# Kernel tuning notes

Hardware: AMD Instinct MI355X
Metric: run time of the kernel (lower is better)

## Reference

```python
import jax, jax.numpy as jnp
import numpy as np

_SAMPLING_EPS = 1e-5
_NEG_INF = -jnp.inf


def _apply_min_p(logits, min_p):
    # probs >= min_p * max_prob are kept (vLLM apply_min_p)
    probs = jax.nn.softmax(logits, axis=-1)
    max_p = jnp.max(probs, axis=-1, keepdims=True)
    keep = probs >= (min_p[:, None] * max_p)
    return jnp.where(keep, logits, _NEG_INF)


def _apply_top_k_top_p(logits, top_k, top_p):
    # One descending sort serves both filters (mirrors vLLM topk/topp kernel).
    T, V = logits.shape
    sorted_l = jnp.sort(logits, axis=-1)[:, ::-1]  # [T, V] descending
    # top-k threshold: k-th largest logit; top_k <= 0 means disabled
    k = jnp.where(top_k <= 0, V, jnp.clip(top_k, 1, V)).astype(jnp.int32)
    kth = jnp.take_along_axis(sorted_l, (k - 1)[:, None], axis=-1)  # [T, 1]
    # top-p: keep smallest prefix whose prob mass reaches top_p (first token always kept)
    probs = jax.nn.softmax(sorted_l, axis=-1)
    cum = jnp.cumsum(probs, axis=-1)
    keep_p = (cum - probs) < top_p[:, None]
    pth = jnp.min(jnp.where(keep_p, sorted_l, jnp.inf), axis=-1, keepdims=True)
    keep = (logits >= kth) & (logits >= pth)
    return jnp.where(keep, logits, _NEG_INF)


def _gather_logprobs(logprobs, num_logprobs, token_ids):
    # vLLM gather_logprobs: topk + sampled-token logprob + rank
    topk_lp, topk_idx = jax.lax.top_k(logprobs, num_logprobs)  # [T, K]
    tok = token_ids[:, None]  # [T, 1]
    tok_lp = jnp.take_along_axis(logprobs, tok, axis=-1)  # [T, 1]
    ranks = jnp.sum(logprobs >= tok_lp, axis=-1).astype(jnp.int32)  # [T]
    indices = jnp.concatenate([tok, topk_idx], axis=1).astype(jnp.int32)
    lps = jnp.concatenate([tok_lp, topk_lp], axis=1)
    return indices, lps, ranks


def setup_inputs() -> dict:
    key = jax.random.key(0)
    k1, k2, k3, k4, k5, k6 = jax.random.split(key, 6)
    T, V = 256, 128256
    logits = jax.random.normal(k1, (T, V), dtype=jnp.float32)
    temperature = 0.2 + 1.3 * jax.random.uniform(k2, (T,), dtype=jnp.float32)
    # every 8th request is greedy (temperature < _SAMPLING_EPS path)
    temperature = jnp.where(jnp.arange(T) % 8 == 0, 0.0, temperature)
    min_p = 0.05 * jax.random.uniform(k3, (T,), dtype=jnp.float32)
    top_p = 0.5 + 0.5 * jax.random.uniform(k4, (T,), dtype=jnp.float32)
    top_k = jax.random.randint(k5, (T,), 0, 64, dtype=jnp.int32)
    u = jax.random.uniform(k6, (T, V), dtype=jnp.float32, minval=1e-10, maxval=1.0)
    return {"logits": logits, "temperature": temperature, "min_p": min_p,
            "top_p": top_p, "top_k": top_k, "u": u, "num_logprobs": 20}


def reference(logits, temperature, min_p, top_p, top_k, u, num_logprobs):
    logits = logits.astype(jnp.float32)
    # logprobs computed on raw (pre-temperature) logits, as in vLLM
    raw_logprobs = jax.nn.log_softmax(logits, axis=-1)
    # greedy path
    greedy = jnp.argmax(logits, axis=-1)
    # random path: temperature -> min_p -> top-k/top-p -> gumbel-max sample
    is_greedy = temperature < _SAMPLING_EPS
    safe_temp = jnp.where(is_greedy, 1.0, temperature)  # rows with temp<eps use greedy anyway
    l = logits / safe_temp[:, None]
    l = _apply_min_p(l, min_p)
    l = _apply_top_k_top_p(l, top_k, top_p)
    gumbel = -jnp.log(-jnp.log(u))  # u in (0,1)
    random_sampled = jnp.argmax(l + gumbel, axis=-1)
    sampled = jnp.where(is_greedy, greedy, random_sampled)
    indices, lps, ranks = _gather_logprobs(raw_logprobs, num_logprobs, sampled)
    sampled_token_ids = sampled.astype(jnp.int32)[:, None]  # [T, 1]
    return sampled_token_ids, indices, lps, ranks
```

## Files before the change

kernel.cpp:

```cpp
#include <hip/hip_runtime.h>
#include <math.h>

#define TPB 1024
#define TPBS 256
#define NS 8
#define NBINS 512
#define CAP 2048
#define NSEL 64
#define MBINS 1024
#define MWIN 16.0f
#define WIN 2.0f
#define SLCAP 1024

typedef unsigned long long u64t;

__device__ __forceinline__ unsigned int ordAsc(float v) {
  unsigned int b = __float_as_uint(v);
  return (b & 0x80000000u) ? ~b : (b | 0x80000000u);
}
__device__ __forceinline__ float ordInv(unsigned int o) {
  return __uint_as_float((o & 0x80000000u) ? (o & 0x7fffffffu) : ~o);
}
__device__ __forceinline__ unsigned int fkeyDesc(float v) { return ~ordAsc(v); }
__device__ __forceinline__ float fkeyInv(unsigned int kd) { return ordInv(~kd); }
__device__ __forceinline__ u64t mkMaxKey(float v, int idx) {
  return ((u64t)ordAsc(v) << 32) | (unsigned int)(~(unsigned int)idx);
}

__device__ __forceinline__ float blockSumF(float v, float* sred) {
  #pragma unroll
  for (int o = 32; o > 0; o >>= 1) v += __shfl_down(v, o, 64);
  int wid = threadIdx.x >> 6, lane = threadIdx.x & 63, nw = blockDim.x >> 6;
  __syncthreads();
  if (lane == 0) sred[wid] = v;
  __syncthreads();
// ... 92 lines not shown
        __syncthreads();
        lds[tid] = key;
        __syncthreads();
        partner = lds[tid ^ j];
      } else {
        partner = __shfl_xor((unsigned long long)key, (int)j, 64);
      }
      bool up = ((tid & k) == 0);
      bool lower = ((tid & j) == 0);
      bool keepSmaller = (up == lower);
      bool pSmaller = (partner < key);
      if (keepSmaller == pSmaller) key = partner;
    }
  }
  __syncthreads();
  lds[tid] = key;
  __syncthreads();
  return key;
}

__global__ __launch_bounds__(TPBS) void k1_max(const float* __restrict__ logits,
                                               u64t* __restrict__ maxes,
                                               int* __restrict__ ccnt,
                                               u64t* __restrict__ mass, int V) {
  const int row = blockIdx.y, s = blockIdx.x, tid = threadIdx.x;
  {
    const int per = MBINS / NS;
    u64t* m = mass + (size_t)row * MBINS + s * per;
    for (int b = tid; b < per; b += TPBS) m[b] = 0ull;
    if (s == 0 && tid == 0) ccnt[row] = 0;
  }
  const float* x = logits + (size_t)row * V;
  const int V4 = V >> 2;
  const float4* x4 = (const float4*)x;
  const int a4 = (int)(((long long)V4 * s) / NS), b4 = (int)(((long long)V4 * (s + 1)) / NS);
  u64t best = 0ull;
  for (int i4 = a4 + tid; i4 < b4; i4 += TPBS) {
    float4 v = x4[i4]; int b = i4 << 2;
    u64t k0 = mkMaxKey(v.x, b);     if (k0 > best) best = k0;
    u64t k1 = mkMaxKey(v.y, b + 1); if (k1 > best) best = k1;
    u64t k2 = mkMaxKey(v.z, b + 2); if (k2 > best) best = k2;
    u64t k3 = mkMaxKey(v.w, b + 3); if (k3 > best) best = k3;
  }
  if (s == NS - 1) for (int i = (V4 << 2) + tid; i < V; i += TPBS) {
    u64t k = mkMaxKey(x[i], i); if (k > best) best = k;
  }
  __shared__ u64t sred[16];
  best = blockMaxU64(best, sred);
  if (tid == 0) maxes[row * NS + s] = best;
}

__global__ __launch_bounds__(TPBS) void k2_sums(const float* __restrict__ logits,
    const float* __restrict__ temp_arr, const u64t* __restrict__ maxes,
    float* __restrict__ s0_ws, float* __restrict__ sl_ws,
    int* __restrict__ ccnt, u64t* __restrict__ cand, int V) {
  const int row = blockIdx.y, s = blockIdx.x, tid = threadIdx.x;
  __shared__ u64t smax[NS];
  __shared__ float sredF[16];
  __shared__ u64t lcand[SLCAP];
  __shared__ int lcnt, lbase;
  if (tid < NS) smax[tid] = maxes[row * NS + tid];
  if (tid == 0) lcnt = 0;
  __syncthreads();
  u64t mk = smax[0];
  for (int w = 1; w < NS; ++w) { u64t t = smax[w]; if (t > mk) mk = t; }
  const float m0 = ordInv((unsigned int)(mk >> 32));
  const float temp = temp_arr[row];
  const bool greedy = (temp < 1e-5f);
  const float st = greedy ? 1.0f : temp;
  const float ml = m0 / st;
  const float wlo = m0 - WIN;
  const float* x = logits + (size_t)row * V;
  const int V4 = V >> 2;
  const float4* x4 = (const float4*)x;
  const int a4 = (int)(((long long)V4 * s) / NS), b4 = (int)(((long long)V4 * (s + 1)) / NS);
  float s0 = 0.f, sl = 0.f;
  auto body = [&](float vv, int gi) {
    s0 += expf(vv - m0);
    if (!greedy) sl += expf(vv / st - ml);
    if (vv >= wlo) {
      int pos = atomicAdd(&lcnt, 1);
      if (pos < SLCAP) lcand[pos] = ((u64t)fkeyDesc(vv) << 32) | (unsigned int)gi;
    }
  };
  for (int i4 = a4 + tid; i4 < b4; i4 += TPBS) {
    float4 v = x4[i4]; int b = i4 << 2;
    body(v.x, b); body(v.y, b + 1); body(v.z, b + 2); body(v.w, b + 3);
  }
  if (s == NS - 1) for (int i = (V4 << 2) + tid; i < V; i += TPBS) body(x[i], i);
  float r0 = blockSumF(s0, sredF);
  float rl = blockSumF(sl, sredF);
  if (tid == 0) {
    s0_ws[row * NS + s] = r0; sl_ws[row * NS + s] = rl;
    int c = lcnt;
    int add = (c > SLCAP) ? (c + CAP + 1) : c;
    lbase = atomicAdd(&ccnt[row], add);
  }
  __syncthreads();
  int c = lcnt < SLCAP ? lcnt : SLCAP;
  int base = lbase;
  for (int j = tid; j < c; j += TPBS) {
    int pos = base + j;
    if (pos < CAP) cand[(size_t)row * CAP + pos] = lcand[j];
  }
}

__global__ __launch_bounds__(TPBS) void k4_sp(const float* __restrict__ logits,
    const float* __restrict__ temp_arr, const float* __restrict__ minp_arr,
    const int* __restrict__ topk_arr, const u64t* __restrict__ maxes,
    const float* __restrict__ sl_ws, float* __restrict__ sp_ws,
    int* __restrict__ ck_ws, u64t* __restrict__ mass, int V) {
  const int row = blockIdx.y, s = blockIdx.x, tid = threadIdx.x;
  const float temp = temp_arr[row];
  if (temp < 1e-5f) {
    if (tid == 0) { sp_ws[row * NS + s] = 0.f; ck_ws[row * NS + s] = 0; }
    return;
  }
  __shared__ u64t smax[NS];
  __shared__ float ssl[NS];
  __shared__ float sredF[16];
  __shared__ int sredI[16];
  __shared__ u64t lmass[MBINS];
  const bool deep = (topk_arr[row] <= 0);
  if (tid < NS) { smax[tid] = maxes[row * NS + tid]; ssl[tid] = sl_ws[row * NS + tid]; }
  if (deep) for (int b = tid; b < MBINS; b += TPBS) lmass[b] = 0ull;
  __syncthreads();
  u64t mk = smax[0];
  for (int w = 1; w < NS; ++w) { u64t t = smax[w]; if (t > mk) mk = t; }
  float S = ssl[0];
  for (int w = 1; w < NS; ++w) S += ssl[w];
  const float m0 = ordInv((unsigned int)(mk >> 32));
  const float st = temp;
  const float ml = m0 / st;
  const float minp = minp_arr[row];
  const float rhs = minp * (1.0f / S);
  const float rhsS = rhs * S;
  const float rhsHi = rhsS * (1.0f + 1e-6f);
  const float rhsLo = rhsS * (1.0f - 1e-6f);
  auto keepTest = [&](float e) -> bool {
    if (e > rhsHi) return true;
    if (e < rhsLo) return false;
    return (e / S) >= rhs;
  };
  const float scaleM = (float)MBINS / MWIN;
  const float* x = logits + (size_t)row * V;
  const int V4 = V >> 2;
  const float4* x4 = (const float4*)x;
  const int a4 = (int)(((long long)V4 * s) / NS), b4 = (int)(((long long)V4 * (s + 1)) / NS);
  float sp = 0.f; int ck = 0;
  auto body = [&](float vv) {
    float l = vv / st;
    float e = expf(l - ml);
    if (keepTest(e)) {
      sp += e; ck++;
      if (deep) {
        float fm = (m0 - vv) * scaleM;
        if (fm < (float)MBINS)
          atomicAdd(&lmass[(int)fm], (u64t)((double)e * 4294967296.0));
      }
    }
  };
  for (int i4 = a4 + tid; i4 < b4; i4 += TPBS) {
    float4 v = x4[i4];
    body(v.x); body(v.y); body(v.z); body(v.w);
  }
  if (s == NS - 1) for (int i = (V4 << 2) + tid; i < V; i += TPBS) body(x[i]);
  float rp = blockSumF(sp, sredF);
  int rc = blockSumI(ck, sredI);
  if (tid == 0) { sp_ws[row * NS + s] = rp; ck_ws[row * NS + s] = rc; }
  if (deep) {
    __syncthreads();
    for (int b = tid; b < MBINS; b += TPBS) {
      u64t m = lmass[b];
      if (m) atomicAdd(&mass[(size_t)row * MBINS + b], m);
    }
  }
}

__global__ __launch_bounds__(TPB) void k5_final(const float* __restrict__ logits,
    const float* __restrict__ temp_arr, const float* __restrict__ minp_arr,
    const float* __restrict__ topp_arr, const int* __restrict__ topk_arr,
    const float* __restrict__ u_arr, const u64t* __restrict__ maxes,
    const float* __restrict__ s0_ws, const float* __restrict__ sl_ws,
    const float* __restrict__ sp_ws, const int* __restrict__ ck_ws,
    const int* __restrict__ ccnt, const u64t* __restrict__ cand,
    const u64t* __restrict__ mass, float* __restrict__ w_thr,
    float* __restrict__ out, int T, int V, int NL) {
  __shared__ u64t keyA[CAP];
  __shared__ u64t keyB[CAP];
  __shared__ float pvals[CAP];
  __shared__ int fh[NBINS];
  __shared__ float sredF[16];
  __shared__ int sredI[16];
  __shared__ u64t smax[NS];
  __shared__ float sp0[NS], spl[NS], spsp[NS];
  __shared__ int spck[NS];
  __shared__ float sh_thresh, sh_toklp;
  __shared__ double sh_seed;
  __shared__ int sh_cnt, sh_bp;

  const int row = blockIdx.x;
  const int tid = threadIdx.x;
  const float* x  = logits + (size_t)row * V;
  const float* uu = u_arr  + (size_t)row * V;
  const float temp = temp_arr[row];
  const float minp = minp_arr[row];
  const float topp = topp_arr[row];
  const int   topk = topk_arr[row];
  const bool greedy = (temp < 1e-5f);
  const float st = greedy ? 1.0f : temp;
  const int V4 = V >> 2;
  const float4* x4 = (const float4*)x;

  if (tid < NS) {
    smax[tid] = maxes[row * NS + tid];
    sp0[tid] = s0_ws[row * NS + tid];
    spl[tid] = sl_ws[row * NS + tid];
    spsp[tid] = sp_ws[row * NS + tid];
    spck[tid] = ck_ws[row * NS + tid];
  }
  __syncthreads();
  u64t mk = smax[0];
  for (int w = 1; w < NS; ++w) { u64t t = smax[w]; if (t > mk) mk = t; }
  const float m0 = ordInv((unsigned int)(mk >> 32));
  const int gidx = (int)(~(unsigned int)mk);
  float S0 = sp0[0], S = spl[0], Sp = spsp[0];
  int ck = spck[0];
  for (int w = 1; w < NS; ++w) { S0 += sp0[w]; S += spl[w]; Sp += spsp[w]; ck += spck[w]; }
  const float ml = m0 / st;
  const float logS0 = logf(S0);
  const float rhs = minp * (1.0f / S);
  const float rhsS = rhs * S;
  const float rhsHi = rhsS * (1.0f + 1e-6f);
  const float rhsLo = rhsS * (1.0f - 1e-6f);
  auto keepTest = [&](float e) -> bool {
    if (e > rhsHi) return true;
    if (e < rhsLo) return false;
    return (e / S) >= rhs;
  };
  const bool deep = (!greedy && topk <= 0);

  int cc = ccnt[row];
  int Cact = cc < CAP ? cc : CAP;
  int need = NSEL;
  if (topk > need) need = topk;
  if (need > CAP / 2) need = CAP / 2;
  if (need > V) need = V;
  bool fb = (cc > CAP) || (Cact < need);
  if (!fb) {
    for (int j = tid; j < Cact; j += TPB) keyA[j] = cand[(size_t)row * CAP + j];
  } else {
    const float bS = (float)NBINS / MWIN;
    for (int b = tid; b < NBINS; b += TPB) fh[b] = 0;
    if (tid == 0) sh_cnt = 0;
    __syncthreads();
    auto hb = [&](float vv) {
      float fbv = (m0 - vv) * bS;
      if (fbv < (float)NBINS) atomicAdd(&fh[(int)fbv], 1);
    };
    for (int i4 = tid; i4 < V4; i4 += TPB) { float4 v = x4[i4]; hb(v.x); hb(v.y); hb(v.z); hb(v.w); }
    for (int i = (V4 << 2) + tid; i < V; i += TPB) hb(x[i]);
    __syncthreads();
    if (tid == 0) {
      int cum = 0, B = -1;
      for (int b = 0; b < NBINS; ++b) { cum += fh[b]; if (cum >= need) { B = b; break; } }
      if (B < 0) B = NBINS - 1;
      sh_bp = B;
    }
    __syncthreads();
    const int B = sh_bp;
    auto cb = [&](float vv, int gi) {
      float fbv = (m0 - vv) * bS;
      if (fbv < (float)NBINS && (int)fbv <= B) {
        int pos = atomicAdd(&sh_cnt, 1);
        if (pos < CAP) keyA[pos] = ((u64t)fkeyDesc(vv) << 32) | (unsigned int)gi;
      }
    };
    for (int i4 = tid; i4 < V4; i4 += TPB) { float4 v = x4[i4]; int b = i4 << 2; cb(v.x, b); cb(v.y, b + 1); cb(v.z, b + 2); cb(v.w, b + 3); }
    for (int i = (V4 << 2) + tid; i < V; i += TPB) cb(x[i], i);
    __syncthreads();
    Cact = sh_cnt < CAP ? sh_cnt : CAP;
  }
  __syncthreads();
  if (Cact <= 1024) {
    u64t ka = (tid < Cact) ? keyA[tid] : ~0ull;
    ka = bitonicReg1024(ka, keyA);
    u64t kb;
    if (tid < Cact) {
      float xv = fkeyInv((unsigned int)(ka >> 32));
      float lp = (xv - m0) - logS0;
      kb = ((u64t)fkeyDesc(lp) << 32) | (ka & 0xffffffffu);
    } else kb = ~0ull;
    bitonicReg1024(kb, keyB);
  } else {
    int n = 128; while (n < Cact) n <<= 1;
    for (int i = Cact + tid; i < n; i += TPB) keyA[i] = ~0ull;
    __syncthreads();
    bitonicSortN(keyA, n);
    for (int j = tid; j < n; j += TPB) {
      if (j < Cact) {
        u64t ka = keyA[j];
        float xv = fkeyInv((unsigned int)(ka >> 32));
        float lp = (xv - m0) - logS0;
        keyB[j] = ((u64t)fkeyDesc(lp) << 32) | (ka & 0xffffffffu);
      } else keyB[j] = ~0ull;
    }
    bitonicSortN(keyB, n);
  }

  int sampled = -1;
  if (greedy) {
    sampled = gidx;
  } else if (topk > 0) {
    if (tid == 0) {
      int k = topk; if (k > V) k = V; if (k > CAP) k = CAP;
      int jp = 0; float cum = 0.f;
      for (int j = 0; j < k; ++j) {
        float pj = 0.f;
        if (j < ck && j < Cact) {
          float xv = fkeyInv((unsigned int)(keyA[j] >> 32));
          pj = expf(xv / st - ml) / Sp;
        }
        cum += pj;
        float ex = cum - pj;
        if (ex < topp) jp = j;
      }
      float thr;
      if (jp < ck && jp < Cact) {
        float xv = fkeyInv((unsigned int)(keyA[jp] >> 32));
        thr = xv / st;
      } else thr = -INFINITY;
      sh_thresh = thr;
    }
    __syncthreads();
    const float thr = sh_thresh;
    float bm = -INFINITY; int bi = 0x7fffffff;
    for (int j = tid; j < Cact; j += TPB) {
      u64t ka = keyA[j];
      float xv = fkeyInv((unsigned int)(ka >> 32));
      int gi = (int)(ka & 0xffffffffu);
      float l = xv / st;
      float e = expf(l - ml);
      if (keepTest(e) && l >= thr) {
        float uv = uu[gi];
        float g = -logf(-logf(uv));
        float val = l + g;
        if (val > bm || (val == bm && gi < bi)) { bm = val; bi = gi; }
      }
    }
    blockArgMaxF(bm, bi, sredF, sredI);
    sampled = bi;
  } else {
    u64t mh = 0;
    if (tid < MBINS) { mh = mass[(size_t)row * MBINS + tid]; keyA[tid] = mh; }
    __syncthreads();
    for (int off = 1; off < MBINS; off <<= 1) {
      u64t add = (tid < MBINS && tid >= off) ? keyA[tid - off] : 0ull;
      __syncthreads();
      if (tid < MBINS) keyA[tid] += add;
      __syncthreads();
    }
    const double TP = (double)topp * (double)Sp;
    int q = -1; u64t myexcl = 0;
    if (tid < MBINS && mh > 0ull) {
      u64t excl = keyA[tid] - mh;
      if ((double)excl * (1.0 / 4294967296.0) < TP) { q = tid; myexcl = excl; }
    }
    int bp = blockMaxI(q, sredI);
    if (bp >= 0 && tid == bp) sh_seed = (double)myexcl * (1.0 / 4294967296.0);
    if (bp < 0 && tid == 0) sh_seed = 0.0;
    __syncthreads();
    float thr;
    if (bp < 0) {
      thr = -INFINITY;
    } else {
      const float scaleM = (float)MBINS / MWIN;
      if (tid == 0) sh_cnt = 0;
      __syncthreads();
      auto bodyC = [&](float vv, int gi) {
        float fm = (m0 - vv) * scaleM;
        if (fm < (float)MBINS && (int)fm == bp) {
          float l = vv / st;
          float e = expf(l - ml);
          if (keepTest(e)) {
            int pos = atomicAdd(&sh_cnt, 1);
            if (pos < CAP) keyA[pos] = ((u64t)fkeyDesc(vv) << 32) | (unsigned int)gi;
          }
        }
      };
      for (int i4 = tid; i4 < V4; i4 += TPB) { float4 v = x4[i4]; int b = i4 << 2; bodyC(v.x, b); bodyC(v.y, b + 1); bodyC(v.z, b + 2); bodyC(v.w, b + 3); }
      for (int i = (V4 << 2) + tid; i < V; i += TPB) bodyC(x[i], i);
      __syncthreads();
      int C5 = sh_cnt < CAP ? sh_cnt : CAP;
      if (C5 <= 1024) {
        u64t kc = (tid < C5) ? keyA[tid] : ~0ull;
        bitonicReg1024(kc, keyA);
      } else {
        int n5 = 128; while (n5 < C5) n5 <<= 1;
        for (int i = C5 + tid; i < n5; i += TPB) keyA[i] = ~0ull;
        __syncthreads();
        bitonicSortN(keyA, n5);
      }
      for (int j = tid; j < C5; j += TPB) {
        float xv = fkeyInv((unsigned int)(keyA[j] >> 32));
        pvals[j] = expf(xv / st - ml) / Sp;
      }
      __syncthreads();
      if (tid == 0) {
        float cum = (float)(sh_seed / (double)Sp);
        float lastVal = fkeyInv((unsigned int)(keyA[0] >> 32));
        for (int j = 0; j < C5; ++j) {
          float pj = pvals[j];
          cum += pj;
          float ex = cum - pj;
          if (ex < topp) lastVal = fkeyInv((unsigned int)(keyA[j] >> 32));
        }
        sh_thresh = lastVal / st;
      }
      __syncthreads();
      thr = sh_thresh;
    }
    if (tid == 0) w_thr[row] = thr;
  }

  if (!deep) {
    if (tid == 0) sh_toklp = (x[sampled] - m0) - logS0;
    __syncthreads();
    const float toklp = sh_toklp;
    int rc = 0;
    for (int j = tid; j < Cact; j += TPB) {
      float xv = fkeyInv((unsigned int)(keyA[j] >> 32));
      float lp = (xv - m0) - logS0;
      if (lp >= toklp) rc++;
    }
    int rank = blockSumI(rc, sredI);
    float* o_samp = out;
    float* o_idx  = out + T;
    float* o_lps  = out + T + (size_t)T * (NL + 1);
    float* o_rank = out + T + (size_t)2 * T * (NL + 1);
    if (tid == 0) {
      o_samp[row] = (float)sampled;
      o_idx[(size_t)row * (NL + 1)] = (float)sampled;
      o_lps[(size_t)row * (NL + 1)] = toklp;
      o_rank[row] = (float)rank;
    }
  }
  {
    float* o_idx  = out + T;
    float* o_lps  = out + T + (size_t)T * (NL + 1);
    for (int j = tid; j < NL; j += TPB) {
      u64t kb = keyB[j];
      o_idx[(size_t)row * (NL + 1) + 1 + j] = (float)(unsigned int)(kb & 0xffffffffu);
      o_lps[(size_t)row * (NL + 1) + 1 + j] = fkeyInv((unsigned int)(kb >> 32));
    }
  }
}

__global__ __launch_bounds__(TPBS) void k6_gumbel(const float* __restrict__ logits,
    const float* __restrict__ temp_arr, const float* __restrict__ minp_arr,
    const int* __restrict__ topk_arr, const float* __restrict__ u_arr,
    const u64t* __restrict__ maxes, const float* __restrict__ sl_ws,
    const float* __restrict__ w_thr, u64t* __restrict__ gkey, int V) {
  const int row = blockIdx.y, s = blockIdx.x, tid = threadIdx.x;
  const float temp = temp_arr[row];
  if (temp < 1e-5f || topk_arr[row] > 0) return;
  __shared__ u64t smax[NS];
  __shared__ float ssl[NS];
  __shared__ float sredF[16];
  __shared__ int sredI[16];
  if (tid < NS) { smax[tid] = maxes[row * NS + tid]; ssl[tid] = sl_ws[row * NS + tid]; }
  __syncthreads();
  u64t mk = smax[0];
  for (int w = 1; w < NS; ++w) { u64t t = smax[w]; if (t > mk) mk = t; }
  float S = ssl[0];
  for (int w = 1; w < NS; ++w) S += ssl[w];
  const float m0 = ordInv((unsigned int)(mk >> 32));
  const float st = temp;
// ... 448 lines not shown
  }
  for (int j = tid; j < NL; j += TPB) {
    u64t kb = keyB[j];
    o_idx[(size_t)row * (NL + 1) + 1 + j] = (float)(unsigned int)(kb & 0xffffffffu);
    o_lps[(size_t)row * (NL + 1) + 1 + j] = fkeyInv((unsigned int)(kb >> 32));
  }
}

extern "C" void kernel_launch(void* const* d_in, const int* in_sizes, int n_in,
                              void* d_out, int out_size, void* d_ws, size_t ws_size,
                              hipStream_t stream) {
  const float* logits = (const float*)d_in[0];
  const float* temp   = (const float*)d_in[1];
  const float* minp   = (const float*)d_in[2];
  const float* topp   = (const float*)d_in[3];
  const int*   topk   = (const int*)d_in[4];
  const float* u      = (const float*)d_in[5];
  const int T  = in_sizes[1];
  const int V  = in_sizes[0] / T;
  const int NL = (out_size / T - 4) / 2;

  size_t off = 0;
  char* base = (char*)d_ws;
  u64t*  w_maxes = (u64t*)(base + off); off += (size_t)T * NS * 8;
  float* w_s0    = (float*)(base + off); off += (size_t)T * NS * 4;
  float* w_sl    = (float*)(base + off); off += (size_t)T * NS * 4;
  float* w_sp    = (float*)(base + off); off += (size_t)T * NS * 4;
  int*   w_ck    = (int*)(base + off);   off += (size_t)T * NS * 4;
  int*   w_ccnt  = (int*)(base + off);   off += ((size_t)T * 4 + 7) & ~(size_t)7;
  u64t*  w_cand  = (u64t*)(base + off);  off += (size_t)T * CAP * 8;
  u64t*  w_mass  = (u64t*)(base + off);  off += (size_t)T * MBINS * 8;
  float* w_thr   = (float*)(base + off); off += ((size_t)T * 4 + 7) & ~(size_t)7;
  u64t*  w_gkey  = (u64t*)(base + off);  off += (size_t)T * NS * 8;

  if (off > ws_size) {
    sampler_mono<<<T, TPB, 0, stream>>>(logits, temp, minp, topp, topk, u,
                                        (float*)d_out, T, V, NL);
    return;
  }

  dim3 gS(NS, T);
  k1_max<<<gS, TPBS, 0, stream>>>(logits, w_maxes, w_ccnt, w_mass, V);
  k2_sums<<<gS, TPBS, 0, stream>>>(logits, temp, w_maxes, w_s0, w_sl, w_ccnt, w_cand, V);
  k4_sp<<<gS, TPBS, 0, stream>>>(logits, temp, minp, topk, w_maxes, w_sl, w_sp, w_ck, w_mass, V);
  k5_final<<<T, TPB, 0, stream>>>(logits, temp, minp, topp, topk, u, w_maxes,
                                  w_s0, w_sl, w_sp, w_ck, w_ccnt, w_cand, w_mass, w_thr,
                                  (float*)d_out, T, V, NL);
  k6_gumbel<<<gS, TPBS, 0, stream>>>(logits, temp, minp, topk, u, w_maxes, w_sl,
                                     w_thr, w_gkey, V);
  k7_deepfin<<<T, TPB, 0, stream>>>(logits, temp, topk, w_gkey, w_s0, w_maxes,
                                    (float*)d_out, T, V, NL);
}
```

Before: 232.1 us.

## Fuse min-p mass pass into sums kernel and split deep top-p collection across blocks

Removes the separate k4_sp pass over the logits. The min-p kept mass, count and deep mass histogram are now computed inside the sums kernel, using the normalizer that is only known later. Values near the min-p boundary are written to a small global band buffer and resolved exactly in k5_final, with a full-row rescan fallback when the band overflows. The single-block full-row scan in k5_final that collected the top-p boundary bin is replaced by a multi-block collect kernel plus a small threshold kernel. This adds launches and global atomics in exchange for one fewer full read of the logits and better parallelism.

```diff
diff --git a/kernel.cpp b/kernel.cpp
--- a/kernel.cpp
+++ b/kernel.cpp
@@ -11,6 +11,7 @@
 #define MWIN 16.0f
 #define WIN 2.0f
 #define SLCAP 1024
+#define BANDCAP 64
 
 typedef unsigned long long u64t;
 
@@ -149,13 +150,14 @@
 __global__ __launch_bounds__(TPBS) void k1_max(const float* __restrict__ logits,
                                                u64t* __restrict__ maxes,
                                                int* __restrict__ ccnt,
+                                               int* __restrict__ bandcnt,
                                                u64t* __restrict__ mass, int V) {
   const int row = blockIdx.y, s = blockIdx.x, tid = threadIdx.x;
   {
     const int per = MBINS / NS;
     u64t* m = mass + (size_t)row * MBINS + s * per;
     for (int b = tid; b < per; b += TPBS) m[b] = 0ull;
-    if (s == 0 && tid == 0) ccnt[row] = 0;
+    if (s == 0 && tid == 0) { ccnt[row] = 0; bandcnt[row] = 0; }
   }
   const float* x = logits + (size_t)row * V;
   const int V4 = V >> 2;
@@ -177,34 +179,63 @@
   if (tid == 0) maxes[row * NS + s] = best;
 }
 
-__global__ __launch_bounds__(TPBS) void k2_sums(const float* __restrict__ logits,
-    const float* __restrict__ temp_arr, const u64t* __restrict__ maxes,
+__global__ __launch_bounds__(TPBS) void k2_all(const float* __restrict__ logits,
+    const float* __restrict__ temp_arr, const float* __restrict__ minp_arr,
+    const int* __restrict__ topk_arr, const u64t* __restrict__ maxes,
     float* __restrict__ s0_ws, float* __restrict__ sl_ws,
-    int* __restrict__ ccnt, u64t* __restrict__ cand, int V) {
+    float* __restrict__ sp_ws, int* __restrict__ ck_ws,
+    int* __restrict__ ccnt, u64t* __restrict__ cand,
+    int* __restrict__ bandcnt, u64t* __restrict__ band,
+    u64t* __restrict__ mass, int V) {
   const int row = blockIdx.y, s = blockIdx.x, tid = threadIdx.x;
   __shared__ u64t smax[NS];
   __shared__ float sredF[16];
+  __shared__ int sredI[16];
   __shared__ u64t lcand[SLCAP];
+  __shared__ u64t lmass[MBINS];
   __shared__ int lcnt, lbase;
+  const float temp = temp_arr[row];
+  const bool greedy = (temp < 1e-5f);
+  const int topk = topk_arr[row];
+  const bool deep = (!greedy && topk <= 0);
   if (tid < NS) smax[tid] = maxes[row * NS + tid];
   if (tid == 0) lcnt = 0;
+  if (deep) for (int b = tid; b < MBINS; b += TPBS) lmass[b] = 0ull;
   __syncthreads();
   u64t mk = smax[0];
   for (int w = 1; w < NS; ++w) { u64t t = smax[w]; if (t > mk) mk = t; }
   const float m0 = ordInv((unsigned int)(mk >> 32));
-  const float temp = temp_arr[row];
-  const bool greedy = (temp < 1e-5f);
   const float st = greedy ? 1.0f : temp;
   const float ml = m0 / st;
   const float wlo = m0 - WIN;
+  const float minp = minp_arr[row];
+  const float bHi = minp * (1.0f + 4e-6f);
+  const float bLo = minp * (1.0f - 4e-6f);
+  const float scaleM = (float)MBINS / MWIN;
   const float* x = logits + (size_t)row * V;
   const int V4 = V >> 2;
   const float4* x4 = (const float4*)x;
   const int a4 = (int)(((long long)V4 * s) / NS), b4 = (int)(((long long)V4 * (s + 1)) / NS);
-  float s0 = 0.f, sl = 0.f;
+  float s0 = 0.f, sl = 0.f, sp = 0.f; int ckp = 0;
   auto body = [&](float vv, int gi) {
     s0 += expf(vv - m0);
-    if (!greedy) sl += expf(vv / st - ml);
+    if (!greedy) {
+      float l = vv / st;
+      float e = expf(l - ml);
+      sl += e;
+      if (minp <= 0.f || e > bHi) {
+        sp += e; ckp++;
+        if (deep) {
+          float fm = (m0 - vv) * scaleM;
+          if (fm < (float)MBINS)
+            atomicAdd(&lmass[(int)fm], (u64t)((double)e * 4294967296.0));
+        }
+      } else if (e >= bLo) {
+        int pos = atomicAdd(&bandcnt[row], 1);
+        if (pos < BANDCAP)
+          band[(size_t)row * BANDCAP + pos] = ((u64t)(unsigned int)gi << 32) | __float_as_uint(vv);
+      }
+    }
     if (vv >= wlo) {
       int pos = atomicAdd(&lcnt, 1);
       if (pos < SLCAP) lcand[pos] = ((u64t)fkeyDesc(vv) << 32) | (unsigned int)gi;
@@ -217,8 +248,11 @@
   if (s == NS - 1) for (int i = (V4 << 2) + tid; i < V; i += TPBS) body(x[i], i);
   float r0 = blockSumF(s0, sredF);
   float rl = blockSumF(sl, sredF);
+  float rp = blockSumF(sp, sredF);
+  int rc = blockSumI(ckp, sredI);
   if (tid == 0) {
     s0_ws[row * NS + s] = r0; sl_ws[row * NS + s] = rl;
+    sp_ws[row * NS + s] = rp; ck_ws[row * NS + s] = rc;
     int c = lcnt;
     int add = (c > SLCAP) ? (c + CAP + 1) : c;
     lbase = atomicAdd(&ccnt[row], add);
@@ -230,27 +264,329 @@
     int pos = base + j;
     if (pos < CAP) cand[(size_t)row * CAP + pos] = lcand[j];
   }
-}
-
-__global__ __launch_bounds__(TPBS) void k4_sp(const float* __restrict__ logits,
+  if (deep) {
+    for (int b = tid; b < MBINS; b += TPBS) {
+      u64t m = lmass[b];
+      if (m) atomicAdd(&mass[(size_t)row * MBINS + b], m);
+    }
+  }
+}
+
+__global__ __launch_bounds__(TPB) void k5_final(const float* __restrict__ logits,
+    const float* __restrict__ temp_arr, const float* __restrict__ minp_arr,
+    const float* __restrict__ topp_arr, const int* __restrict__ topk_arr,
+    const float* __restrict__ u_arr, const u64t* __restrict__ maxes,
+    const float* __restrict__ s0_ws, const float* __restrict__ sl_ws,
+    const float* __restrict__ sp_ws, const int* __restrict__ ck_ws,
+    int* __restrict__ ccnt, const u64t* __restrict__ cand,
+    const u64t* __restrict__ mass, const u64t* __restrict__ band,
+    const int* __restrict__ bandcnt, float* __restrict__ w_thr,
+    int* __restrict__ w_bpM, double* __restrict__ w_seed, float* __restrict__ w_spD,
+    float* __restrict__ out, int T, int V, int NL) {
+  __shared__ u64t keyA[CAP];
+  __shared__ u64t keyB[CAP];
+  __shared__ int fh[NBINS];
+  __shared__ float sredF[16];
+  __shared__ int sredI[16];
+  __shared__ u64t smax[NS];
+  __shared__ float sp0[NS], spl[NS], spsp[NS];
+  __shared__ int spck[NS];
+  __shared__ float sh_thresh, sh_toklp, sh_spAdd;
+  __shared__ double sh_seed;
+  __shared__ int sh_cnt, sh_bp, sh_bCnt, sh_ckAdd;
+  __shared__ u64t sh_bKeys[BANDCAP];
+  __shared__ u64t sh_bMass[BANDCAP];
+  __shared__ int  sh_bBin[BANDCAP];
+
+  const int row = blockIdx.x;
+  const int tid = threadIdx.x;
+  const float* x  = logits + (size_t)row * V;
+  const float* uu = u_arr  + (size_t)row * V;
+  const float temp = temp_arr[row];
+  const float minp = minp_arr[row];
+  const float topp = topp_arr[row];
+  const int   topk = topk_arr[row];
+  const bool greedy = (temp < 1e-5f);
+  const float st = greedy ? 1.0f : temp;
+  const int V4 = V >> 2;
+  const float4* x4 = (const float4*)x;
+
+  if (tid < NS) {
+    smax[tid] = maxes[row * NS + tid];
+    sp0[tid] = s0_ws[row * NS + tid];
+    spl[tid] = sl_ws[row * NS + tid];
+    spsp[tid] = sp_ws[row * NS + tid];
+    spck[tid] = ck_ws[row * NS + tid];
+  }
+  __syncthreads();
+  u64t mk = smax[0];
+  for (int w = 1; w < NS; ++w) { u64t t = smax[w]; if (t > mk) mk = t; }
+  const float m0 = ordInv((unsigned int)(mk >> 32));
+  const int gidx = (int)(~(unsigned int)mk);
+  float S0 = sp0[0], S = spl[0], Sp = spsp[0];
+  int ck = spck[0];
+  for (int w = 1; w < NS; ++w) { S0 += sp0[w]; S += spl[w]; Sp += spsp[w]; ck += spck[w]; }
+  const float ml = m0 / st;
+  const float logS0 = logf(S0);
+  const float rhs = minp * (1.0f / S);
+  const float rhsS = rhs * S;
+  const float rhsHi = rhsS * (1.0f + 1e-6f);
+  const float rhsLo = rhsS * (1.0f - 1e-6f);
+  auto keepTest = [&](float e) -> bool {
+    if (e > rhsHi) return true;
+    if (e < rhsLo) return false;
+    return (e / S) >= rhs;
+  };
+  const bool deep = (!greedy && topk <= 0);
+  const float scaleM = (float)MBINS / MWIN;
+
+  const int bandTotal = greedy ? 0 : bandcnt[row];
+  const bool bandOv = bandTotal > BANDCAP;
+  if (tid == 0) { sh_bCnt = 0; sh_spAdd = 0.f; sh_ckAdd = 0; }
+  __syncthreads();
+  if (!greedy && !bandOv && bandTotal > 0 && minp > 0.f) {
+    if (tid == 0) {
+      for (int i = 0; i < bandTotal; ++i) sh_bKeys[i] = band[(size_t)row * BANDCAP + i];
+      for (int i = 1; i < bandTotal; ++i) {
+        u64t k = sh_bKeys[i]; int j = i - 1;
+        while (j >= 0 && sh_bKeys[j] > k) { sh_bKeys[j + 1] = sh_bKeys[j]; j--; }
+        sh_bKeys[j + 1] = k;
+      }
+      float spAdd = 0.f; int ckAdd = 0, bc = 0;
+      for (int i = 0; i < bandTotal; ++i) {
+        float vv = __uint_as_float((unsigned int)(sh_bKeys[i] & 0xffffffffu));
+        float l = vv / st; float e = expf(l - ml);
+        if ((e / S) >= rhs) {
+          spAdd += e; ckAdd++;
+          if (deep) {
+            float fm = (m0 - vv) * scaleM;
+            if (fm < (float)MBINS) { sh_bBin[bc] = (int)fm; sh_bMass[bc] = (u64t)((double)e * 4294967296.0); bc++; }
+          }
+        }
+      }
+      sh_spAdd = spAdd; sh_ckAdd = ckAdd; sh_bCnt = bc;
+    }
+    __syncthreads();
+    Sp += sh_spAdd; ck += sh_ckAdd;
+  } else if (!greedy && bandOv) {
+    float sp2 = 0.f; int ck2 = 0;
+    auto bodyR = [&](float vv) {
+      float l = vv / st; float e = expf(l - ml);
+      if (keepTest(e)) { sp2 += e; ck2++; }
+    };
+    for (int i4 = tid; i4 < V4; i4 += TPB) { float4 v = x4[i4]; bodyR(v.x); bodyR(v.y); bodyR(v.z); bodyR(v.w); }
+    for (int i = (V4 << 2) + tid; i < V; i += TPB) bodyR(x[i]);
+    Sp = blockSumF(sp2, sredF);
+    ck = blockSumI(ck2, sredI);
+  }
+
+  int cc = ccnt[row];
+  int Cact = cc < CAP ? cc : CAP;
+  int need = NSEL;
+  if (topk > need) need = topk;
+  if (need > CAP / 2) need = CAP / 2;
+  if (need > V) need = V;
+  bool fb = (cc > CAP) || (Cact < need);
+  if (!fb) {
+    for (int j = tid; j < Cact; j += TPB) keyA[j] = cand[(size_t)row * CAP + j];
+  } else {
+    const float bS = (float)NBINS / MWIN;
+    for (int b = tid; b < NBINS; b += TPB) fh[b] = 0;
+    if (tid == 0) sh_cnt = 0;
+    __syncthreads();
+    auto hb = [&](float vv) {
+      float fbv = (m0 - vv) * bS;
+      if (fbv < (float)NBINS) atomicAdd(&fh[(int)fbv], 1);
+    };
+    for (int i4 = tid; i4 < V4; i4 += TPB) { float4 v = x4[i4]; hb(v.x); hb(v.y); hb(v.z); hb(v.w); }
+    for (int i = (V4 << 2) + tid; i < V; i += TPB) hb(x[i]);
+    __syncthreads();
+    if (tid == 0) {
+      int cum = 0, B = -1;
+      for (int b = 0; b < NBINS; ++b) { cum += fh[b]; if (cum >= need) { B = b; break; } }
+      if (B < 0) B = NBINS - 1;
+      sh_bp = B;
+    }
+    __syncthreads();
+    const int B = sh_bp;
+    auto cb = [&](float vv, int gi) {
+      float fbv = (m0 - vv) * bS;
+      if (fbv < (float)NBINS && (int)fbv <= B) {
+        int pos = atomicAdd(&sh_cnt, 1);
+        if (pos < CAP) keyA[pos] = ((u64t)fkeyDesc(vv) << 32) | (unsigned int)gi;
+      }
+    };
+    for (int i4 = tid; i4 < V4; i4 += TPB) { float4 v = x4[i4]; int b = i4 << 2; cb(v.x, b); cb(v.y, b + 1); cb(v.z, b + 2); cb(v.w, b + 3); }
+    for (int i = (V4 << 2) + tid; i < V; i += TPB) cb(x[i], i);
+    __syncthreads();
+    Cact = sh_cnt < CAP ? sh_cnt : CAP;
+  }
+  __syncthreads();
+  if (Cact <= 1024) {
+    u64t ka = (tid < Cact) ? keyA[tid] : ~0ull;
+    ka = bitonicReg1024(ka, keyA);
+    u64t kb;
+    if (tid < Cact) {
+      float xv = fkeyInv((unsigned int)(ka >> 32));
+      float lp = (xv - m0) - logS0;
+      kb = ((u64t)fkeyDesc(lp) << 32) | (ka & 0xffffffffu);
+    } else kb = ~0ull;
+    bitonicReg1024(kb, keyB);
+  } else {
+    int n = 128; while (n < Cact) n <<= 1;
+    for (int i = Cact + tid; i < n; i += TPB) keyA[i] = ~0ull;
+    __syncthreads();
+    bitonicSortN(keyA, n);
+    for (int j = tid; j < n; j += TPB) {
+      if (j < Cact) {
+        u64t ka = keyA[j];
+        float xv = fkeyInv((unsigned int)(ka >> 32));
+        float lp = (xv - m0) - logS0;
+        keyB[j] = ((u64t)fkeyDesc(lp) << 32) | (ka & 0xffffffffu);
+      } else keyB[j] = ~0ull;
+    }
+    bitonicSortN(keyB, n);
+  }
+
+  int sampled = -1;
+  if (greedy) {
+    sampled = gidx;
+  } else if (topk > 0) {
+    if (tid == 0) {
+      int k = topk; if (k > V) k = V; if (k > CAP) k = CAP;
+      int jp = 0; float cum = 0.f;
+      for (int j = 0; j < k; ++j) {
+        float pj = 0.f;
+        if (j < ck && j < Cact) {
+          float xv = fkeyInv((unsigned int)(keyA[j] >> 32));
+          pj = expf(xv / st - ml) / Sp;
+        }
+        cum += pj;
+        float ex = cum - pj;
+        if (ex < topp) jp = j;
+      }
+      float thr;
+      if (jp < ck && jp < Cact) {
+        float xv = fkeyInv((unsigned int)(keyA[jp] >> 32));
+        thr = xv / st;
+      } else thr = -INFINITY;
+      sh_thresh = thr;
+    }
+    __syncthreads();
+    const float thr = sh_thresh;
+    float bm = -INFINITY; int bi = 0x7fffffff;
+    for (int j = tid; j < Cact; j += TPB) {
+      u64t ka = keyA[j];
+      float xv = fkeyInv((unsigned int)(ka >> 32));
+      int gi = (int)(ka & 0xffffffffu);
+      float l = xv / st;
+      float e = expf(l - ml);
+      if (keepTest(e) && l >= thr) {
+        float uv = uu[gi];
+        float g = -logf(-logf(uv));
+        float val = l + g;
+        if (val > bm || (val == bm && gi < bi)) { bm = val; bi = gi; }
+      }
+    }
+    blockArgMaxF(bm, bi, sredF, sredI);
+    sampled = bi;
+  } else {
+    if (!bandOv) {
+      if (tid < MBINS) {
+        u64t m = mass[(size_t)row * MBINS + tid];
+        int bc = sh_bCnt;
+        for (int j = 0; j < bc; ++j) if (sh_bBin[j] == tid) m += sh_bMass[j];
+        keyA[tid] = m;
+      }
+    } else {
+      for (int b = tid; b < MBINS; b += TPB) keyA[b] = 0ull;
+      __syncthreads();
+      auto bodyM = [&](float vv) {
+        float l = vv / st; float e = expf(l - ml);
+        if (keepTest(e)) {
+          float fm = (m0 - vv) * scaleM;
+          if (fm < (float)MBINS) atomicAdd(&keyA[(int)fm], (u64t)((double)e * 4294967296.0));
+        }
+      };
+      for (int i4 = tid; i4 < V4; i4 += TPB) { float4 v = x4[i4]; bodyM(v.x); bodyM(v.y); bodyM(v.z); bodyM(v.w); }
+      for (int i = (V4 << 2) + tid; i < V; i += TPB) bodyM(x[i]);
+    }
+    __syncthreads();
+    u64t mh = (tid < MBINS) ? keyA[tid] : 0ull;
+    for (int off = 1; off < MBINS; off <<= 1) {
+      u64t add = (tid < MBINS && tid >= off) ? keyA[tid - off] : 0ull;
+      __syncthreads();
+      if (tid < MBINS) keyA[tid] += add;
+      __syncthreads();
+    }
+    const double TP = (double)topp * (double)Sp;
+    int q = -1; u64t myexcl = 0;
+    if (tid < MBINS && mh > 0ull) {
+      u64t excl = keyA[tid] - mh;
+      if ((double)excl * (1.0 / 4294967296.0) < TP) { q = tid; myexcl = excl; }
+    }
+    int bp = blockMaxI(q, sredI);
+    if (bp >= 0 && tid == bp) sh_seed = (double)myexcl * (1.0 / 4294967296.0);
+    if (bp < 0 && tid == 0) sh_seed = 0.0;
+    __syncthreads();
+    if (tid == 0) {
+      w_bpM[row] = bp;
+      w_seed[row] = sh_seed;
+      w_spD[row] = Sp;
+      ccnt[row] = 0;
+      if (bp < 0) w_thr[row] = -INFINITY;
+    }
+  }
+
+  if (!deep) {
+    if (tid == 0) sh_toklp = (x[sampled] - m0) - logS0;
+    __syncthreads();
+    const float toklp = sh_toklp;
+    int rc = 0;
+    for (int j = tid; j < Cact; j += TPB) {
+      float xv = fkeyInv((unsigned int)(keyA[j] >> 32));
+      float lp = (xv - m0) - logS0;
+      if (lp >= toklp) rc++;
+    }
+    int rank = blockSumI(rc, sredI);
+    float* o_samp = out;
+    float* o_idx  = out + T;
+    float* o_lps  = out + T + (size_t)T * (NL + 1);
+    float* o_rank = out + T + (size_t)2 * T * (NL + 1);
+    if (tid == 0) {
+      o_samp[row] = (float)sampled;
+      o_idx[(size_t)row * (NL + 1)] = (float)sampled;
+      o_lps[(size_t)row * (NL + 1)] = toklp;
+      o_rank[row] = (float)rank;
+    }
+  }
+  {
+    float* o_idx  = out + T;
+    float* o_lps  = out + T + (size_t)T * (NL + 1);
+    for (int j = tid; j < NL; j += TPB) {
+      u64t kb = keyB[j];
+      o_idx[(size_t)row * (NL + 1) + 1 + j] = (float)(unsigned int)(kb & 0xffffffffu);
+      o_lps[(size_t)row * (NL + 1) + 1 + j] = fkeyInv((unsigned int)(kb >> 32));
+    }
+  }
+}
+
+__global__ __launch_bounds__(TPBS) void k5b_collect(const float* __restrict__ logits,
     const float* __restrict__ temp_arr, const float* __restrict__ minp_arr,
     const int* __restrict__ topk_arr, const u64t* __restrict__ maxes,
-    const float* __restrict__ sl_ws, float* __restrict__ sp_ws,
-    int* __restrict__ ck_ws, u64t* __restrict__ mass, int V) {
+    const float* __restrict__ sl_ws, const int* __restrict__ w_bpM,
+    int* __restrict__ ccnt, u64t* __restrict__ cand, int V) {
   const int row = blockIdx.y, s = blockIdx.x, tid = threadIdx.x;
   const float temp = temp_arr[row];
-  if (temp < 1e-5f) {
-    if (tid == 0) { sp_ws[row * NS + s] = 0.f; ck_ws[row * NS + s] = 0; }
-    return;
-  }
+  if (temp < 1e-5f || topk_arr[row] > 0) return;
+  const int bp = w_bpM[row];
+  if (bp < 0) return;
   __shared__ u64t smax[NS];
   __shared__ float ssl[NS];
-  __shared__ float sredF[16];
-  __shared__ int sredI[16];
-  __shared__ u64t lmass[MBINS];
-  const bool deep = (topk_arr[row] <= 0);
+  __shared__ u64t lcand[SLCAP];
+  __shared__ int lcnt, lbase;
   if (tid < NS) { smax[tid] = maxes[row * NS + tid]; ssl[tid] = sl_ws[row * NS + tid]; }
-  if (deep) for (int b = tid; b < MBINS; b += TPBS) lmass[b] = 0ull;
+  if (tid == 0) lcnt = 0;
   __syncthreads();
   u64t mk = smax[0];
   for (int w = 1; w < NS; ++w) { u64t t = smax[w]; if (t > mk) mk = t; }
@@ -274,312 +610,87 @@
   const int V4 = V >> 2;
   const float4* x4 = (const float4*)x;
   const int a4 = (int)(((long long)V4 * s) / NS), b4 = (int)(((long long)V4 * (s + 1)) / NS);
-  float sp = 0.f; int ck = 0;
-  auto body = [&](float vv) {
-    float l = vv / st;
-    float e = expf(l - ml);
-    if (keepTest(e)) {
-      sp += e; ck++;
-      if (deep) {
-        float fm = (m0 - vv) * scaleM;
-        if (fm < (float)MBINS)
-          atomicAdd(&lmass[(int)fm], (u64t)((double)e * 4294967296.0));
+  auto body = [&](float vv, int gi) {
+    float fm = (m0 - vv) * scaleM;
+    if (fm < (float)MBINS && (int)fm == bp) {
+      float l = vv / st;
+      float e = expf(l - ml);
+      if (keepTest(e)) {
+        int pos = atomicAdd(&lcnt, 1);
+        if (pos < SLCAP) lcand[pos] = ((u64t)fkeyDesc(vv) << 32) | (unsigned int)gi;
       }
     }
   };
   for (int i4 = a4 + tid; i4 < b4; i4 += TPBS) {
-    float4 v = x4[i4];
-    body(v.x); body(v.y); body(v.z); body(v.w);
-  }
-  if (s == NS - 1) for (int i = (V4 << 2) + tid; i < V; i += TPBS) body(x[i]);
-  float rp = blockSumF(sp, sredF);
-  int rc = blockSumI(ck, sredI);
-  if (tid == 0) { sp_ws[row * NS + s] = rp; ck_ws[row * NS + s] = rc; }
-  if (deep) {
-    __syncthreads();
-    for (int b = tid; b < MBINS; b += TPBS) {
-      u64t m = lmass[b];
-      if (m) atomicAdd(&mass[(size_t)row * MBINS + b], m);
-    }
-  }
-}
-
-__global__ __launch_bounds__(TPB) void k5_final(const float* __restrict__ logits,
-    const float* __restrict__ temp_arr, const float* __restrict__ minp_arr,
+    float4 v = x4[i4]; int b = i4 << 2;
+    body(v.x, b); body(v.y, b + 1); body(v.z, b + 2); body(v.w, b + 3);
+  }
+  if (s == NS - 1) for (int i = (V4 << 2) + tid; i < V; i += TPBS) body(x[i], i);
+  __syncthreads();
+  if (tid == 0) {
+    int c = lcnt < SLCAP ? lcnt : SLCAP;
+    lbase = atomicAdd(&ccnt[row], c);
+  }
+  __syncthreads();
+  int c = lcnt < SLCAP ? lcnt : SLCAP;
+  int base = lbase;
+  for (int j = tid; j < c; j += TPBS) {
+    int pos = base + j;
+    if (pos < CAP) cand[(size_t)row * CAP + pos] = lcand[j];
+  }
+}
+
+__global__ __launch_bounds__(TPB) void k5c_thr(const float* __restrict__ temp_arr,
     const float* __restrict__ topp_arr, const int* __restrict__ topk_arr,
-    const float* __restrict__ u_arr, const u64t* __restrict__ maxes,
-    const float* __restrict__ s0_ws, const float* __restrict__ sl_ws,
-    const float* __restrict__ sp_ws, const int* __restrict__ ck_ws,
+    const u64t* __restrict__ maxes, const int* __restrict__ w_bpM,
     const int* __restrict__ ccnt, const u64t* __restrict__ cand,
-    const u64t* __restrict__ mass, float* __restrict__ w_thr,
-    float* __restrict__ out, int T, int V, int NL) {
+    const float* __restrict__ w_spD, const double* __restrict__ w_seed,
+    float* __restrict__ w_thr) {
+  const int row = blockIdx.x, tid = threadIdx.x;
+  const float temp = temp_arr[row];
+  if (temp < 1e-5f || topk_arr[row] > 0) return;
+  const int bp = w_bpM[row];
+  if (bp < 0) return;
   __shared__ u64t keyA[CAP];
-  __shared__ u64t keyB[CAP];
   __shared__ float pvals[CAP];
-  __shared__ int fh[NBINS];
-  __shared__ float sredF[16];
-  __shared__ int sredI[16];
   __shared__ u64t smax[NS];
-  __shared__ float sp0[NS], spl[NS], spsp[NS];
-  __shared__ int spck[NS];
-  __shared__ float sh_thresh, sh_toklp;
-  __shared__ double sh_seed;
-  __shared__ int sh_cnt, sh_bp;
-
-  const int row = blockIdx.x;
-  const int tid = threadIdx.x;
-  const float* x  = logits + (size_t)row * V;
-  const float* uu = u_arr  + (size_t)row * V;
-  const float temp = temp_arr[row];
-  const float minp = minp_arr[row];
-  const float topp = topp_arr[row];
-  const int   topk = topk_arr[row];
-  const bool greedy = (temp < 1e-5f);
-  const float st = greedy ? 1.0f : temp;
-  const int V4 = V >> 2;
-  const float4* x4 = (const float4*)x;
-
-  if (tid < NS) {
-    smax[tid] = maxes[row * NS + tid];
-    sp0[tid] = s0_ws[row * NS + tid];
-    spl[tid] = sl_ws[row * NS + tid];
-    spsp[tid] = sp_ws[row * NS + tid];
-    spck[tid] = ck_ws[row * NS + tid];
-  }
+  if (tid < NS) smax[tid] = maxes[row * NS + tid];
   __syncthreads();
   u64t mk = smax[0];
   for (int w = 1; w < NS; ++w) { u64t t = smax[w]; if (t > mk) mk = t; }
   const float m0 = ordInv((unsigned int)(mk >> 32));
-  const int gidx = (int)(~(unsigned int)mk);
-  float S0 = sp0[0], S = spl[0], Sp = spsp[0];
-  int ck = spck[0];
-  for (int w = 1; w < NS; ++w) { S0 += sp0[w]; S += spl[w]; Sp += spsp[w]; ck += spck[w]; }
+  const float st = temp;
   const float ml = m0 / st;
-  const float logS0 = logf(S0);
-  const float rhs = minp * (1.0f / S);
-  const float rhsS = rhs * S;
-  const float rhsHi = rhsS * (1.0f + 1e-6f);
-  const float rhsLo = rhsS * (1.0f - 1e-6f);
-  auto keepTest = [&](float e) -> bool {
-    if (e > rhsHi) return true;
-    if (e < rhsLo) return false;
-    return (e / S) >= rhs;
-  };
-  const bool deep = (!greedy && topk <= 0);
-
+  const float Sp = w_spD[row];
+  const double seed = w_seed[row];
+  const float topp = topp_arr[row];
   int cc = ccnt[row];
-  int Cact = cc < CAP ? cc : CAP;
-  int need = NSEL;
-  if (topk > need) need = topk;
-  if (need > CAP / 2) need = CAP / 2;
-  if (need > V) need = V;
-  bool fb = (cc > CAP) || (Cact < need);
-  if (!fb) {
-    for (int j = tid; j < Cact; j += TPB) keyA[j] = cand[(size_t)row * CAP + j];
+  int C5 = cc < CAP ? cc : CAP;
+  if (C5 <= 1024) {
+    u64t kc = (tid < C5) ? cand[(size_t)row * CAP + tid] : ~0ull;
+    bitonicReg1024(kc, keyA);
   } else {
-    const float bS = (float)NBINS / MWIN;
-    for (int b = tid; b < NBINS; b += TPB) fh[b] = 0;
-    if (tid == 0) sh_cnt = 0;
-    __syncthreads();
-    auto hb = [&](float vv) {
-      float fbv = (m0 - vv) * bS;
-      if (fbv < (float)NBINS) atomicAdd(&fh[(int)fbv], 1);
-    };
-    for (int i4 = tid; i4 < V4; i4 += TPB) { float4 v = x4[i4]; hb(v.x); hb(v.y); hb(v.z); hb(v.w); }
-    for (int i = (V4 << 2) + tid; i < V; i += TPB) hb(x[i]);
-    __syncthreads();
-    if (tid == 0) {
-      int cum = 0, B = -1;
-      for (int b = 0; b < NBINS; ++b) { cum += fh[b]; if (cum >= need) { B = b; break; } }
-      if (B < 0) B = NBINS - 1;
-      sh_bp = B;
-    }
-    __syncthreads();
-    const int B = sh_bp;
-    auto cb = [&](float vv, int gi) {
-      float fbv = (m0 - vv) * bS;
-      if (fbv < (float)NBINS && (int)fbv <= B) {
-        int pos = atomicAdd(&sh_cnt, 1);
-        if (pos < CAP) keyA[pos] = ((u64t)fkeyDesc(vv) << 32) | (unsigned int)gi;
-      }
-    };
-    for (int i4 = tid; i4 < V4; i4 += TPB) { float4 v = x4[i4]; int b = i4 << 2; cb(v.x, b); cb(v.y, b + 1); cb(v.z, b + 2); cb(v.w, b + 3); }
-    for (int i = (V4 << 2) + tid; i < V; i += TPB) cb(x[i], i);
-    __syncthreads();
-    Cact = sh_cnt < CAP ? sh_cnt : CAP;
-  }
-  __syncthreads();
-  if (Cact <= 1024) {
-    u64t ka = (tid < Cact) ? keyA[tid] : ~0ull;
-    ka = bitonicReg1024(ka, keyA);
-    u64t kb;
-    if (tid < Cact) {
-      float xv = fkeyInv((unsigned int)(ka >> 32));
-      float lp = (xv - m0) - logS0;
-      kb = ((u64t)fkeyDesc(lp) << 32) | (ka & 0xffffffffu);
-    } else kb = ~0ull;
-    bitonicReg1024(kb, keyB);
-  } else {
-    int n = 128; while (n < Cact) n <<= 1;
-    for (int i = Cact + tid; i < n; i += TPB) keyA[i] = ~0ull;
-    __syncthreads();
-    bitonicSortN(keyA, n);
-    for (int j = tid; j < n; j += TPB) {
-      if (j < Cact) {
-        u64t ka = keyA[j];
-        float xv = fkeyInv((unsigned int)(ka >> 32));
-        float lp = (xv - m0) - logS0;
-        keyB[j] = ((u64t)fkeyDesc(lp) << 32) | (ka & 0xffffffffu);
-      } else keyB[j] = ~0ull;
-    }
-    bitonicSortN(keyB, n);
-  }
-
-  int sampled = -1;
-  if (greedy) {
-    sampled = gidx;
-  } else if (topk > 0) {
-    if (tid == 0) {
-      int k = topk; if (k > V) k = V; if (k > CAP) k = CAP;
-      int jp = 0; float cum = 0.f;
-      for (int j = 0; j < k; ++j) {
-        float pj = 0.f;
-        if (j < ck && j < Cact) {
-          float xv = fkeyInv((unsigned int)(keyA[j] >> 32));
-          pj = expf(xv / st - ml) / Sp;
-        }
-        cum += pj;
-        float ex = cum - pj;
-        if (ex < topp) jp = j;
-      }
-      float thr;
-      if (jp < ck && jp < Cact) {
-        float xv = fkeyInv((unsigned int)(keyA[jp] >> 32));
-        thr = xv / st;
-      } else thr = -INFINITY;
-      sh_thresh = thr;
-    }
-    __syncthreads();
-    const float thr = sh_thresh;
-    float bm = -INFINITY; int bi = 0x7fffffff;
-    for (int j = tid; j < Cact; j += TPB) {
-      u64t ka = keyA[j];
-      float xv = fkeyInv((unsigned int)(ka >> 32));
-      int gi = (int)(ka & 0xffffffffu);
-      float l = xv / st;
-      float e = expf(l - ml);
-      if (keepTest(e) && l >= thr) {
-        float uv = uu[gi];
-        float g = -logf(-logf(uv));
-        float val = l + g;
-        if (val > bm || (val == bm && gi < bi)) { bm = val; bi = gi; }
-      }
-    }
-    blockArgMaxF(bm, bi, sredF, sredI);
-    sampled = bi;
-  } else {
-    u64t mh = 0;
-    if (tid < MBINS) { mh = mass[(size_t)row * MBINS + tid]; keyA[tid] = mh; }
-    __syncthreads();
-    for (int off = 1; off < MBINS; off <<= 1) {
-      u64t add = (tid < MBINS && tid >= off) ? keyA[tid - off] : 0ull;
-      __syncthreads();
-      if (tid < MBINS) keyA[tid] += add;
-      __syncthreads();
-    }
-    const double TP = (double)topp * (double)Sp;
-    int q = -1; u64t myexcl = 0;
-    if (tid < MBINS && mh > 0ull) {
-      u64t excl = keyA[tid] - mh;
-      if ((double)excl * (1.0 / 4294967296.0) < TP) { q = tid; myexcl = excl; }
-    }
-    int bp = blockMaxI(q, sredI);
-    if (bp >= 0 && tid == bp) sh_seed = (double)myexcl * (1.0 / 4294967296.0);
-    if (bp < 0 && tid == 0) sh_seed = 0.0;
-    __syncthreads();
-    float thr;
-    if (bp < 0) {
-      thr = -INFINITY;
-    } else {
-      const float scaleM = (float)MBINS / MWIN;
-      if (tid == 0) sh_cnt = 0;
-      __syncthreads();
-      auto bodyC = [&](float vv, int gi) {
-        float fm = (m0 - vv) * scaleM;
-        if (fm < (float)MBINS && (int)fm == bp) {
-          float l = vv / st;
-          float e = expf(l - ml);
-          if (keepTest(e)) {
-            int pos = atomicAdd(&sh_cnt, 1);
-            if (pos < CAP) keyA[pos] = ((u64t)fkeyDesc(vv) << 32) | (unsigned int)gi;
-          }
-        }
-      };
-      for (int i4 = tid; i4 < V4; i4 += TPB) { float4 v = x4[i4]; int b = i4 << 2; bodyC(v.x, b); bodyC(v.y, b + 1); bodyC(v.z, b + 2); bodyC(v.w, b + 3); }
-      for (int i = (V4 << 2) + tid; i < V; i += TPB) bodyC(x[i], i);
-      __syncthreads();
-      int C5 = sh_cnt < CAP ? sh_cnt : CAP;
-      if (C5 <= 1024) {
-        u64t kc = (tid < C5) ? keyA[tid] : ~0ull;
-        bitonicReg1024(kc, keyA);
-      } else {
-        int n5 = 128; while (n5 < C5) n5 <<= 1;
-        for (int i = C5 + tid; i < n5; i += TPB) keyA[i] = ~0ull;
-        __syncthreads();
-        bitonicSortN(keyA, n5);
-      }
-      for (int j = tid; j < C5; j += TPB) {
-        float xv = fkeyInv((unsigned int)(keyA[j] >> 32));
-        pvals[j] = expf(xv / st - ml) / Sp;
-      }
-      __syncthreads();
-      if (tid == 0) {
-        float cum = (float)(sh_seed / (double)Sp);
-        float lastVal = fkeyInv((unsigned int)(keyA[0] >> 32));
-        for (int j = 0; j < C5; ++j) {
-          float pj = pvals[j];
-          cum += pj;
-          float ex = cum - pj;
-          if (ex < topp) lastVal = fkeyInv((unsigned int)(keyA[j] >> 32));
-        }
-        sh_thresh = lastVal / st;
-      }
-      __syncthreads();
-      thr = sh_thresh;
-    }
-    if (tid == 0) w_thr[row] = thr;
-  }
-
-  if (!deep) {
-    if (tid == 0) sh_toklp = (x[sampled] - m0) - logS0;
-    __syncthreads();
-    const float toklp = sh_toklp;
-    int rc = 0;
-    for (int j = tid; j < Cact; j += TPB) {
-      float xv = fkeyInv((unsigned int)(keyA[j] >> 32));
-      float lp = (xv - m0) - logS0;
-      if (lp >= toklp) rc++;
-    }
-    int rank = blockSumI(rc, sredI);
-    float* o_samp = out;
-    float* o_idx  = out + T;
-    float* o_lps  = out + T + (size_t)T * (NL + 1);
-    float* o_rank = out + T + (size_t)2 * T * (NL + 1);
-    if (tid == 0) {
-      o_samp[row] = (float)sampled;
-      o_idx[(size_t)row * (NL + 1)] = (float)sampled;
-      o_lps[(size_t)row * (NL + 1)] = toklp;
-      o_rank[row] = (float)rank;
-    }
-  }
-  {
-    float* o_idx  = out + T;
-    float* o_lps  = out + T + (size_t)T * (NL + 1);
-    for (int j = tid; j < NL; j += TPB) {
-      u64t kb = keyB[j];
-      o_idx[(size_t)row * (NL + 1) + 1 + j] = (float)(unsigned int)(kb & 0xffffffffu);
-      o_lps[(size_t)row * (NL + 1) + 1 + j] = fkeyInv((unsigned int)(kb >> 32));
-    }
+    for (int j = tid; j < CAP; j += TPB)
+      keyA[j] = (j < C5) ? cand[(size_t)row * CAP + j] : ~0ull;
+    int n5 = 128; while (n5 < C5) n5 <<= 1;
+    __syncthreads();
+    bitonicSortN(keyA, n5);
+  }
+  for (int j = tid; j < C5; j += TPB) {
+    float xv = fkeyInv((unsigned int)(keyA[j] >> 32));
+    pvals[j] = expf(xv / st - ml) / Sp;
+  }
+  __syncthreads();
+  if (tid == 0) {
+    float cum = (float)(seed / (double)Sp);
+    float lastVal = fkeyInv((unsigned int)(keyA[0] >> 32));
+    for (int j = 0; j < C5; ++j) {
+      float pj = pvals[j];
+      cum += pj;
+      float ex = cum - pj;
+      if (ex < topp) lastVal = fkeyInv((unsigned int)(keyA[j] >> 32));
+    }
+    w_thr[row] = lastVal / st;
   }
 }
 
@@ -1074,16 +1185,21 @@
 
   size_t off = 0;
   char* base = (char*)d_ws;
-  u64t*  w_maxes = (u64t*)(base + off); off += (size_t)T * NS * 8;
-  float* w_s0    = (float*)(base + off); off += (size_t)T * NS * 4;
-  float* w_sl    = (float*)(base + off); off += (size_t)T * NS * 4;
-  float* w_sp    = (float*)(base + off); off += (size_t)T * NS * 4;
-  int*   w_ck    = (int*)(base + off);   off += (size_t)T * NS * 4;
-  int*   w_ccnt  = (int*)(base + off);   off += ((size_t)T * 4 + 7) & ~(size_t)7;
-  u64t*  w_cand  = (u64t*)(base + off);  off += (size_t)T * CAP * 8;
-  u64t*  w_mass  = (u64t*)(base + off);  off += (size_t)T * MBINS * 8;
-  float* w_thr   = (float*)(base + off); off += ((size_t)T * 4 + 7) & ~(size_t)7;
-  u64t*  w_gkey  = (u64t*)(base + off);  off += (size_t)T * NS * 8;
+  u64t*   w_maxes   = (u64t*)(base + off);   off += (size_t)T * NS * 8;
+  u64t*   w_cand    = (u64t*)(base + off);   off += (size_t)T * CAP * 8;
+  u64t*   w_mass    = (u64t*)(base + off);   off += (size_t)T * MBINS * 8;
+  u64t*   w_gkey    = (u64t*)(base + off);   off += (size_t)T * NS * 8;
+  u64t*   w_band    = (u64t*)(base + off);   off += (size_t)T * BANDCAP * 8;
+  double* w_seed    = (double*)(base + off); off += (size_t)T * 8;
+  float*  w_s0      = (float*)(base + off);  off += (size_t)T * NS * 4;
+  float*  w_sl      = (float*)(base + off);  off += (size_t)T * NS * 4;
+  float*  w_sp      = (float*)(base + off);  off += (size_t)T * NS * 4;
+  int*    w_ck      = (int*)(base + off);    off += (size_t)T * NS * 4;
+  int*    w_ccnt    = (int*)(base + off);    off += (size_t)T * 4;
+  int*    w_bandcnt = (int*)(base + off);    off += (size_t)T * 4;
+  float*  w_thr     = (float*)(base + off);  off += (size_t)T * 4;
+  int*    w_bpM     = (int*)(base + off);    off += (size_t)T * 4;
+  float*  w_spD     = (float*)(base + off);  off += (size_t)T * 4;
 
   if (off > ws_size) {
     sampler_mono<<<T, TPB, 0, stream>>>(logits, temp, minp, topp, topk, u,
@@ -1092,12 +1208,18 @@
   }
 
   dim3 gS(NS, T);
-  k1_max<<<gS, TPBS, 0, stream>>>(logits, w_maxes, w_ccnt, w_mass, V);
-  k2_sums<<<gS, TPBS, 0, stream>>>(logits, temp, w_maxes, w_s0, w_sl, w_ccnt, w_cand, V);
-  k4_sp<<<gS, TPBS, 0, stream>>>(logits, temp, minp, topk, w_maxes, w_sl, w_sp, w_ck, w_mass, V);
+  k1_max<<<gS, TPBS, 0, stream>>>(logits, w_maxes, w_ccnt, w_bandcnt, w_mass, V);
+  k2_all<<<gS, TPBS, 0, stream>>>(logits, temp, minp, topk, w_maxes, w_s0, w_sl,
+                                  w_sp, w_ck, w_ccnt, w_cand, w_bandcnt, w_band,
+                                  w_mass, V);
   k5_final<<<T, TPB, 0, stream>>>(logits, temp, minp, topp, topk, u, w_maxes,
-                                  w_s0, w_sl, w_sp, w_ck, w_ccnt, w_cand, w_mass, w_thr,
+                                  w_s0, w_sl, w_sp, w_ck, w_ccnt, w_cand, w_mass,
+                                  w_band, w_bandcnt, w_thr, w_bpM, w_seed, w_spD,
                                   (float*)d_out, T, V, NL);
+  k5b_collect<<<gS, TPBS, 0, stream>>>(logits, temp, minp, topk, w_maxes, w_sl,
+                                       w_bpM, w_ccnt, w_cand, V);
+  k5c_thr<<<T, TPB, 0, stream>>>(temp, topp, topk, w_maxes, w_bpM, w_ccnt, w_cand,
+                                 w_spD, w_seed, w_thr);
   k6_gumbel<<<gS, TPBS, 0, stream>>>(logits, temp, minp, topk, u, w_maxes, w_sl,
                                      w_thr, w_gkey, V);
   k7_deepfin<<<T, TPB, 0, stream>>>(logits, temp, topk, w_gkey, w_s0, w_maxes,
```

After: 219.8 us. 1.06x faster.
